# Performance work log

Measured on AMD Instinct MI355X. Metric: run time of the kernel, lower is better.

The kernel has to match this reference:

```python
import jax, jax.numpy as jnp
import numpy as np
from functools import partial

TOP_K = 2
LN_EPS = 1e-5


def setup_inputs() -> dict:
    key = jax.random.key(0)
    ks = jax.random.split(key, 4)
    B, T, H, F, E = 2, 2048, 1024, 4096, 8
    hidden_states = jax.random.normal(ks[0], (B, T, H), dtype=jnp.float32)
    # Router weights: original inits to zeros; use small random so routing is non-degenerate.
    router_w = jax.random.normal(ks[1], (E, H), dtype=jnp.float32) * 0.02
    router_b = jnp.zeros((E,), dtype=jnp.float32)
    W1 = jax.random.normal(ks[2], (E, H, F), dtype=jnp.float32) * (1.0 / np.sqrt(H))
    b1 = jnp.zeros((E, F), dtype=jnp.float32)
    W2 = jax.random.normal(ks[3], (E, F, H), dtype=jnp.float32) * (1.0 / np.sqrt(F))
    b2 = jnp.zeros((E, H), dtype=jnp.float32)
    ln_gamma = jnp.ones((H,), dtype=jnp.float32)
    ln_beta = jnp.zeros((H,), dtype=jnp.float32)
    return {"hidden_states": hidden_states, "router_w": router_w, "router_b": router_b,
            "W1": W1, "b1": b1, "W2": W2, "b2": b2,
            "ln_gamma": ln_gamma, "ln_beta": ln_beta}


def _layer_norm(x, gamma, beta):
    mu = jnp.mean(x, axis=-1, keepdims=True)
    var = jnp.var(x, axis=-1, keepdims=True)
    return (x - mu) * jax.lax.rsqrt(var + LN_EPS) * gamma + beta


def _moe_forward(hidden_states, router_w, router_b, W1, b1, W2, b2, ln_gamma, ln_beta):
    B, T, H = hidden_states.shape
    E = router_w.shape[0]
    N = B * T
    x = hidden_states.reshape(N, H)
    # Router (jitter=0.0, eval mode): logits [N, E]
    logits = x @ router_w.T + router_b
    topk_vals, topk_idx = jax.lax.top_k(logits, TOP_K)        # [N, K]
    topk_w = jax.nn.softmax(topk_vals, axis=-1)               # [N, K]
    # Scatter top-k weights into a dense combine matrix [N, E] (zeros elsewhere).
    probs = jnp.zeros((N, E), dtype=x.dtype).at[jnp.arange(N)[:, None], topk_idx].set(topk_w)
    # Per-expert FFN via scan over the (small, fixed) expert axis; each step is one
    # big GEMM over all tokens weighted by that expert's combine prob (0 for
    # tokens not routed to it) — same math as gather/MLP/scatter with no capacity drop.
    def body(acc, params_e):
        Wa, ba, Wb, bb, pe = params_e          # pe: [N]
        h = jax.nn.gelu(x @ Wa + ba, approximate=False)   # [N, F]
        y = h @ Wb + bb                                    # [N, H]
        return acc + y * pe[:, None], None
    out, _ = jax.lax.scan(body, jnp.zeros_like(x), (W1, b1, W2, b2, probs.T))
    out = out.reshape(B, T, H)
    return _layer_norm(out + hidden_states, ln_gamma, ln_beta)


def reference(hidden_states, router_w, router_b, W1, b1, W2, b2, ln_gamma, ln_beta):
    return _moe_forward(hidden_states, router_w, router_b, W1, b1, W2, b2, ln_gamma, ln_beta)
```

## Files before the change

### kernel.cpp

```cpp
#include <hip/hip_runtime.h>
#include <hip/hip_bf16.h>


typedef unsigned short u16;
typedef unsigned int u32;
typedef __attribute__((ext_vector_type(4))) float f32x4;
typedef __attribute__((ext_vector_type(8))) short s16x8;
typedef __attribute__((ext_vector_type(4))) unsigned short u16x4;
typedef __attribute__((ext_vector_type(8))) unsigned short u16x8;

#define GLD16(gp, lp) __builtin_amdgcn_global_load_lds( \
    (const __attribute__((address_space(1))) void*)(gp), \
    (__attribute__((address_space(3))) void*)(lp), 16, 0, 0)

__device__ __forceinline__ u16 f2bf(float f) {
    union { float f; u32 u; } v; v.f = f;
    u32 u = v.u;
    return (u16)((u + 0x7fffu + ((u >> 16) & 1u)) >> 16);
}
__device__ __forceinline__ float bf2f(u16 h) {
    union { u32 u; float f; } v; v.u = ((u32)h) << 16; return v.f;
}

__device__ __forceinline__ float gelu_f(float v) {
    const float u = v * (0.7978845608f + 0.0356774081f * v * v);
    const float t = __expf(-2.0f * u);
    return v * __builtin_amdgcn_rcpf(1.0f + t);
}

__global__ void k_init(int* cc) { if (threadIdx.x < 16) cc[threadIdx.x] = 0; }

__global__ __launch_bounds__(256) void k_pre(
    const float* __restrict__ x, const float* __restrict__ rw, const float* __restrict__ rb,
    u16* __restrict__ xb, int* __restrict__ eidx, float* __restrict__ wgt, int* __restrict__ counts,
    const float* __restrict__ W1, u16* __restrict__ W1t,
    const float* __restrict__ W2, u16* __restrict__ W2t)
{
    __shared__ u16 tl[256 * 128];
    const int id = blockIdx.x;
    const int tid = threadIdx.x;

    if (id >= 1024) {
        const float* s; u16* d; int R, C, r0, c0;
        if (id < 2048) {
            const int id2 = id - 1024;
            const int e = id2 >> 7, rem = id2 & 127;
            const int rt = rem >> 5, ct = rem & 31;
            s = W1 + (size_t)e * 1024 * 4096; d = W1t + (size_t)e * 1024 * 4096;
            R = 1024; C = 4096; r0 = rt * 256; c0 = ct * 128;
        } else {
            const int id3 = id - 2048;
            const int e = id3 >> 7, rem = id3 & 127;
            const int rt = rem >> 3, ct = rem & 7;
            s = W2 + (size_t)e * 4096 * 1024; d = W2t + (size_t)e * 4096 * 1024;
            R = 4096; C = 1024; r0 = rt * 256; c0 = ct * 128;
        }
        const int g = tid >> 5, ln = tid & 31;
        #pragma unroll 4
        for (int it = 0; it < 32; ++it) {
            const int r = it * 8 + g;
            const float4 v = *(const float4*)(s + (size_t)(r0 + r) * C + c0 + ln * 4);
            u16x4 pk;
            pk[0] = f2bf(v.x); pk[1] = f2bf(v.y); pk[2] = f2bf(v.z); pk[3] = f2bf(v.w);
            const int word = r * 32 + (ln ^ (r >> 3));
            *(u16x4*)(&tl[word * 4]) = pk;
        }
        __syncthreads();
        #pragma unroll 2
        for (int it = 0; it < 16; ++it) {
            const int c = it * 8 + g;
            const int cw = c >> 2, ce = c & 3;
            u16x8 o;
            #pragma unroll
            for (int j = 0; j < 8; ++j) {
                const int r = ln * 8 + j;
                const int word = r * 32 + (cw ^ (r >> 3));
                o[j] = tl[word * 4 + ce];
            }
            *(u16x8*)(d + (size_t)(c0 + c) * R + r0 + ln * 8) = o;
        }
        return;
    }

    const int wav = tid >> 6, lane = tid & 63;
    const int t = id * 4 + wav;
    const float* xt = x + (size_t)t * 1024;
    float acc[8] = {0.f,0.f,0.f,0.f,0.f,0.f,0.f,0.f};
    #pragma unroll
    for (int c = 0; c < 4; c++) {
        const int base = c * 256 + lane * 4;
        const float4 xv = *(const float4*)(xt + base);
        ushort4 pk;
        pk.x = f2bf(xv.x); pk.y = f2bf(xv.y); pk.z = f2bf(xv.z); pk.w = f2bf(xv.w);
        *(ushort4*)(xb + (size_t)t * 1024 + base) = pk;
        #pragma unroll
        for (int e = 0; e < 8; e++) {
            const float4 wv = *(const float4*)(rw + e * 1024 + base);
            acc[e] += xv.x * wv.x + xv.y * wv.y + xv.z * wv.z + xv.w * wv.w;
        }
    }
    #pragma unroll
    for (int e = 0; e < 8; e++) {
        #pragma unroll
        for (int s = 32; s; s >>= 1) acc[e] += __shfl_xor(acc[e], s);
    }
    if (lane == 0) {
        float v0 = -3e38f, v1 = -3e38f; int i0 = 0, i1 = 0;
        #pragma unroll
        for (int e = 0; e < 8; e++) {
            const float l = acc[e] + rb[e];
            if (l > v0) { v1 = v0; i1 = i0; v0 = l; i0 = e; }
            else if (l > v1) { v1 = l; i1 = e; }
        }
        const float w0 = 1.0f / (1.0f + expf(v1 - v0));
        eidx[2 * t] = i0; eidx[2 * t + 1] = i1;
        wgt[2 * t] = w0; wgt[2 * t + 1] = 1.0f - w0;
        atomicAdd(&counts[i0], 1); atomicAdd(&counts[i1], 1);
    }
}

__global__ __launch_bounds__(256) void k_place2(
    const int* __restrict__ eidx, const int* __restrict__ counts, int* __restrict__ cursors,
    int* __restrict__ offsets, int* __restrict__ rows, int* __restrict__ pos_of)
{
    int base[8];
    int s = 0;
    #pragma unroll
    for (int e = 0; e < 8; e++) { base[e] = s; s += counts[e]; }
    if (blockIdx.x == 0 && threadIdx.x == 0) {
        #pragma unroll
        for (int e = 0; e < 8; e++) offsets[e] = base[e];
        offsets[8] = s;
    }
    const int a = blockIdx.x * 256 + threadIdx.x;
    const int e = eidx[a];
    const int pos = base[e] + atomicAdd(&cursors[e], 1);
    rows[pos] = a >> 1;
    pos_of[a] = pos;
}

#define STAGE_T(b, k0) { \
    char* ad = (char*)At + (b) * 8192 + wav * 1024; \
    char* bd = (char*)Bt + (b) * 8192 + wav * 1024; \
    GLD16(a_src0 + (k0), ad); \
    GLD16(a_src1 + (k0), ad + 4096); \
    GLD16(b_src0 + (k0), bd); \
    GLD16(b_src1 + (k0), bd + 4096); }

#define COMPUTE_T(b) { \
    const u16* Abp = Ab + (b) * 4096; \
    const u16* Bbp = Bb + (b) * 4096; \
    s16x8 af[4], bfr[4]; \
    _Pragma("unroll") \
    for (int i = 0; i < 4; i++) { \
        af[i]  = *(const s16x8*)(Abp + i * 512); \
        bfr[i] = *(const s16x8*)(Bbp + i * 512); \
    } \
    __builtin_amdgcn_s_setprio(1); \
    _Pragma("unroll") \
    for (int mi = 0; mi < 4; mi++) \
        _Pragma("unroll") \
        for (int ni = 0; ni < 4; ni++) \
            acc[mi][ni] = __builtin_amdgcn_mfma_f32_16x16x32_bf16(af[mi], bfr[ni], acc[mi][ni], 0, 0, 0); \
    __builtin_amdgcn_s_setprio(0); }

#define VMCNT4 asm volatile("s_waitcnt vmcnt(4)" ::: "memory")
#define VMCNT0 asm volatile("s_waitcnt vmcnt(0)" ::: "memory")
#define BAR __builtin_amdgcn_s_barrier()

__global__ __launch_bounds__(256, 4) void k_gemm1(
    const u16* __restrict__ xb, const u16* __restrict__ W1t, const float* __restrict__ b1,
    u16* __restrict__ hbuf, const int* __restrict__ rows, const int* __restrict__ offsets)
{
    const int fid = blockIdx.x;
    const int swz = (fid & 7) * 1024 + (fid >> 3);
    const int y = swz & 31, xx = (swz >> 5) & 31, e = swz >> 10;

    const int off = offsets[e], cnt = offsets[e + 1] - off;
    const int row0 = y * 128;
    if (row0 >= cnt) return;
    const int n0 = xx * 128;
    const int tid = threadIdx.x;
    const int lane = tid & 63, wav = tid >> 6, lane15 = lane & 15;

    __shared__ u16 At[2][128][32];
    __shared__ u16 Bt[2][128][32];

    const int ar0 = tid >> 2;
    const int cl8 = (((tid & 3) ^ ((tid >> 3) & 3))) * 8;
    const int t0 = rows[off + min(row0 + ar0, cnt - 1)];
    const int t1 = rows[off + min(row0 + ar0 + 64, cnt - 1)];
    const u16* a_src0 = xb + (size_t)t0 * 1024 + cl8;
    const u16* a_src1 = xb + (size_t)t1 * 1024 + cl8;
    const u16* b_src0 = W1t + ((size_t)e * 4096 + n0 + ar0) * 1024 + cl8;
    const u16* b_src1 = b_src0 + (size_t)64 * 1024;

    f32x4 acc[4][4] = {};
    const int wr = wav >> 1, wc = wav & 1;
    const int koff = ((lane >> 4) ^ ((lane >> 1) & 3)) * 8;
    const u16* Ab = &At[0][wr * 64 + lane15][koff];
    const u16* Bb = &Bt[0][wc * 64 + lane15][koff];

    STAGE_T(0, 0);
    int b = 0;
    for (int k0 = 32; k0 < 1024; k0 += 32) {
        STAGE_T(b ^ 1, k0);
        VMCNT4;
        BAR;
        COMPUTE_T(b);
        BAR;
        b ^= 1;
    }
    VMCNT0;
    BAR;
    COMPUTE_T(b);

    const int rb4 = (lane >> 4) * 4;
    const int colbase = n0 + wc * 64 + lane15;
    float bias[4];
    #pragma unroll
    for (int ni = 0; ni < 4; ni++) bias[ni] = b1[e * 4096 + colbase + ni * 16];
    #pragma unroll
    for (int mi = 0; mi < 4; mi++) {
        #pragma unroll
        for (int j = 0; j < 4; j++) {
            const int lrow = wr * 64 + mi * 16 + rb4 + j;
            if (row0 + lrow < cnt) {
                const size_t gr = (size_t)(off + row0 + lrow);
                #pragma unroll
                for (int ni = 0; ni < 4; ni++) {
                    const float v = acc[mi][ni][j] + bias[ni];
                    hbuf[gr * 4096 + colbase + ni * 16] = f2bf(gelu_f(v));
                }
            }
        }
    }
}

__global__ __launch_bounds__(256, 4) void k_gemm2(
    const u16* __restrict__ hbuf, const u16* __restrict__ W2t, const float* __restrict__ b2,
    u16* __restrict__ yb, const int* __restrict__ offsets)
{
    const int fid = blockIdx.x;
    const int swz = (fid & 7) * 1024 + (fid >> 3);
    const int y = swz & 31, xx = (swz >> 5) & 7, z = swz >> 8;
    const int e = z >> 2, kq = z & 3;

    const int off = offsets[e], cnt = offsets[e + 1] - off;
    const int row0 = y * 128;
    if (row0 >= cnt) return;
    const int n0 = xx * 128;
    const int tid = threadIdx.x;
    const int lane = tid & 63, wav = tid >> 6, lane15 = lane & 15;
    const int kbase = kq * 1024;

    __shared__ u16 At[2][128][32];
    __shared__ u16 Bt[2][128][32];

    const int ar0 = tid >> 2;
    const int cl8 = (((tid & 3) ^ ((tid >> 3) & 3))) * 8;
    const u16* a_src0 = hbuf + (size_t)(off + min(row0 + ar0, cnt - 1)) * 4096 + kbase + cl8;
    const u16* a_src1 = hbuf + (size_t)(off + min(row0 + ar0 + 64, cnt - 1)) * 4096 + kbase + cl8;
    const u16* b_src0 = W2t + ((size_t)e * 1024 + n0 + ar0) * 4096 + kbase + cl8;
    const u16* b_src1 = b_src0 + (size_t)64 * 4096;

    f32x4 acc[4][4] = {};
    const int wr = wav >> 1, wc = wav & 1;
    const int koff = ((lane >> 4) ^ ((lane >> 1) & 3)) * 8;
    const u16* Ab = &At[0][wr * 64 + lane15][koff];
    const u16* Bb = &Bt[0][wc * 64 + lane15][koff];

    STAGE_T(0, 0);
    int b = 0;
    for (int k0 = 32; k0 < 1024; k0 += 32) {
        STAGE_T(b ^ 1, k0);
        VMCNT4;
        BAR;
        COMPUTE_T(b);
        BAR;
        b ^= 1;
    }
    VMCNT0;
    BAR;
    COMPUTE_T(b);

    u16* yy = yb + (size_t)kq * 8192 * 1024;
    const int rb4 = (lane >> 4) * 4;
    const int colbase = n0 + wc * 64 + lane15;
    float bias[4];
    #pragma unroll
    for (int ni = 0; ni < 4; ni++) bias[ni] = (kq == 0) ? b2[e * 1024 + colbase + ni * 16] : 0.f;
    #pragma unroll
    for (int mi = 0; mi < 4; mi++) {
        #pragma unroll
        for (int j = 0; j < 4; j++) {
            const int lrow = wr * 64 + mi * 16 + rb4 + j;
            if (row0 + lrow < cnt) {
                const size_t gr = (size_t)(off + row0 + lrow);
                #pragma unroll
                for (int ni = 0; ni < 4; ni++)
                    yy[gr * 1024 + colbase + ni * 16] = f2bf(acc[mi][ni][j] + bias[ni]);
            }
        }
    }
}

__global__ __launch_bounds__(256) void k_combine(
    const float* __restrict__ x, const u16* __restrict__ yb,
    const int* __restrict__ pos_of, const float* __restrict__ wgt,
    const float* __restrict__ gamma, const float* __restrict__ beta,
    float* __restrict__ out)
{
    const int t = blockIdx.x;
    const int tid = threadIdx.x;
    const int p0 = pos_of[2 * t], p1 = pos_of[2 * t + 1];
    const float w0 = wgt[2 * t], w1 = wgt[2 * t + 1];
    const int j4 = tid * 4;
    const float4 xv = *(const float4*)(x + (size_t)t * 1024 + j4);
    float s0[4] = {0.f, 0.f, 0.f, 0.f};
    float s1[4] = {0.f, 0.f, 0.f, 0.f};
    #pragma unroll
    for (int kq = 0; kq < 4; kq++) {
        const u16* ybq = yb + (size_t)kq * 8192 * 1024;
        const ushort4 u0 = *(const ushort4*)(ybq + (size_t)p0 * 1024 + j4);
        const ushort4 u1 = *(const ushort4*)(ybq + (size_t)p1 * 1024 + j4);
        s0[0] += bf2f(u0.x); s0[1] += bf2f(u0.y); s0[2] += bf2f(u0.z); s0[3] += bf2f(u0.w);
        s1[0] += bf2f(u1.x); s1[1] += bf2f(u1.y); s1[2] += bf2f(u1.z); s1[3] += bf2f(u1.w);
    }
    float a0 = xv.x + w0 * s0[0] + w1 * s1[0];
    float a1 = xv.y + w0 * s0[1] + w1 * s1[1];
    float a2 = xv.z + w0 * s0[2] + w1 * s1[2];
    float a3 = xv.w + w0 * s0[3] + w1 * s1[3];
    float s = a0 + a1 + a2 + a3;
    float q = a0 * a0 + a1 * a1 + a2 * a2 + a3 * a3;
    #pragma unroll
    for (int o = 32; o; o >>= 1) { s += __shfl_xor(s, o); q += __shfl_xor(q, o); }
    __shared__ float ls[4], lq[4];
    const int wav = tid >> 6, lane = tid & 63;
    if (lane == 0) { ls[wav] = s; lq[wav] = q; }
    __syncthreads();
    s = ls[0] + ls[1] + ls[2] + ls[3];
    q = lq[0] + lq[1] + lq[2] + lq[3];
    const float mu = s * (1.0f / 1024.0f);
    const float var = q * (1.0f / 1024.0f) - mu * mu;
    const float rs = rsqrtf(var + 1e-5f);
    const float4 g = *(const float4*)(gamma + j4);
    const float4 b = *(const float4*)(beta + j4);
    float4 o4;
    o4.x = (a0 - mu) * rs * g.x + b.x;
    o4.y = (a1 - mu) * rs * g.y + b.y;
    o4.z = (a2 - mu) * rs * g.z + b.z;
    o4.w = (a3 - mu) * rs * g.w + b.w;
    *(float4*)(out + (size_t)t * 1024 + j4) = o4;
}

extern "C" void kernel_launch(void* const* d_in, const int* in_sizes, int n_in,
                              void* d_out, int out_size, void* d_ws, size_t ws_size,
                              hipStream_t stream) {
    const float* x     = (const float*)d_in[0];
    const float* rw    = (const float*)d_in[1];
    const float* rb    = (const float*)d_in[2];
    const float* W1    = (const float*)d_in[3];
    const float* b1    = (const float*)d_in[4];
    const float* W2    = (const float*)d_in[5];
    const float* b2    = (const float*)d_in[6];
    const float* gamma = (const float*)d_in[7];
    const float* beta  = (const float*)d_in[8];
    float* out = (float*)d_out;

    char* p = (char*)d_ws;
    auto alloc = [&](size_t bytes) { char* r = p; p += (bytes + 255) & ~(size_t)255; return r; };
    int*   counts  = (int*)alloc(16 * sizeof(int));
    int*   cursors = counts + 8;
    int*   offsets = (int*)alloc(9 * sizeof(int));
    int*   eidx    = (int*)alloc(8192 * sizeof(int));
    float* wgt     = (float*)alloc(8192 * sizeof(float));
    int*   pos_of  = (int*)alloc(8192 * sizeof(int));
    int*   rows    = (int*)alloc(8192 * sizeof(int));
    u16*   xb      = (u16*)alloc((size_t)4096 * 1024 * 2);
    u16*   W1t     = (u16*)alloc((size_t)8 * 4096 * 1024 * 2);
    u16*   W2t     = (u16*)alloc((size_t)8 * 1024 * 4096 * 2);
    u16*   hbuf    = (u16*)alloc((size_t)8192 * 4096 * 2);
    u16* yb = W1t;

    hipLaunchKernelGGL(k_init, dim3(1), dim3(64), 0, stream, counts);
    hipLaunchKernelGGL(k_pre, dim3(3072), dim3(256), 0, stream,
                       x, rw, rb, xb, eidx, wgt, counts, W1, W1t, W2, W2t);
    hipLaunchKernelGGL(k_place2, dim3(32), dim3(256), 0, stream,
                       eidx, counts, cursors, offsets, rows, pos_of);
    hipLaunchKernelGGL(k_gemm1, dim3(8192), dim3(256), 0, stream, xb, W1t, b1, hbuf, rows, offsets);
    hipLaunchKernelGGL(k_gemm2, dim3(8192), dim3(256), 0, stream, hbuf, W2t, b2, yb, offsets);
    hipLaunchKernelGGL(k_combine, dim3(4096), dim3(256), 0, stream, x, yb, pos_of, wgt, gamma, beta, out);
}
```

Measured before the change: 428.3 us.

## Move W2 transpose into GEMM1 launch and drop LDS from weight transposes

The W2 fp32-to-bf16 transpose moves out of the preprocessing kernel and into extra leading blocks of the first GEMM launch, so it can overlap with GEMM1 compute. Both weight transposes now use a register-only scheme: each thread reads 8 strided fp32 values down a column and writes one 16-byte bf16 vector, with no shared-memory staging or barrier. The aim is to hide transpose memory traffic and cut LDS use and barriers. The risk is that the strided per-thread reads are less coalesced, and the transpose blocks compete with GEMM blocks for CUs.

Measured after the change: 449.4 us. +4.9%, slower.

```diff
diff --git a/kernel.cpp b/kernel.cpp
--- a/kernel.cpp
+++ b/kernel.cpp
@@ -6,7 +6,6 @@
 typedef unsigned int u32;
 typedef __attribute__((ext_vector_type(4))) float f32x4;
 typedef __attribute__((ext_vector_type(8))) short s16x8;
-typedef __attribute__((ext_vector_type(4))) unsigned short u16x4;
 typedef __attribute__((ext_vector_type(8))) unsigned short u16x8;
 
 #define GLD16(gp, lp) __builtin_amdgcn_global_load_lds( \
@@ -30,55 +29,38 @@
 
 __global__ void k_init(int* cc) { if (threadIdx.x < 16) cc[threadIdx.x] = 0; }
 
+__device__ __forceinline__ void transp_nolds(
+    const float* __restrict__ s, u16* __restrict__ d, int K, int N, int n0, int k0, int tid)
+{
+    const int n = n0 + tid;
+    #pragma unroll 4
+    for (int c8 = 0; c8 < 8; ++c8) {
+        const int kb = k0 + c8 * 8;
+        float v[8];
+        #pragma unroll
+        for (int j = 0; j < 8; ++j)
+            v[j] = s[(size_t)(kb + j) * N + n];
+        u16x8 o;
+        #pragma unroll
+        for (int j = 0; j < 8; ++j) o[j] = f2bf(v[j]);
+        *(u16x8*)(d + (size_t)n * K + kb) = o;
+    }
+}
+
 __global__ __launch_bounds__(256) void k_pre(
     const float* __restrict__ x, const float* __restrict__ rw, const float* __restrict__ rb,
     u16* __restrict__ xb, int* __restrict__ eidx, float* __restrict__ wgt, int* __restrict__ counts,
-    const float* __restrict__ W1, u16* __restrict__ W1t,
-    const float* __restrict__ W2, u16* __restrict__ W2t)
-{
-    __shared__ u16 tl[256 * 128];
+    const float* __restrict__ W1, u16* __restrict__ W1t)
+{
     const int id = blockIdx.x;
     const int tid = threadIdx.x;
 
     if (id >= 1024) {
-        const float* s; u16* d; int R, C, r0, c0;
-        if (id < 2048) {
-            const int id2 = id - 1024;
-            const int e = id2 >> 7, rem = id2 & 127;
-            const int rt = rem >> 5, ct = rem & 31;
-            s = W1 + (size_t)e * 1024 * 4096; d = W1t + (size_t)e * 1024 * 4096;
-            R = 1024; C = 4096; r0 = rt * 256; c0 = ct * 128;
-        } else {
-            const int id3 = id - 2048;
-            const int e = id3 >> 7, rem = id3 & 127;
-            const int rt = rem >> 3, ct = rem & 7;
-            s = W2 + (size_t)e * 4096 * 1024; d = W2t + (size_t)e * 4096 * 1024;
-            R = 4096; C = 1024; r0 = rt * 256; c0 = ct * 128;
-        }
-        const int g = tid >> 5, ln = tid & 31;
-        #pragma unroll 4
-        for (int it = 0; it < 32; ++it) {
-            const int r = it * 8 + g;
-            const float4 v = *(const float4*)(s + (size_t)(r0 + r) * C + c0 + ln * 4);
-            u16x4 pk;
-            pk[0] = f2bf(v.x); pk[1] = f2bf(v.y); pk[2] = f2bf(v.z); pk[3] = f2bf(v.w);
-            const int word = r * 32 + (ln ^ (r >> 3));
-            *(u16x4*)(&tl[word * 4]) = pk;
-        }
-        __syncthreads();
-        #pragma unroll 2
-        for (int it = 0; it < 16; ++it) {
-            const int c = it * 8 + g;
-            const int cw = c >> 2, ce = c & 3;
-            u16x8 o;
-            #pragma unroll
-            for (int j = 0; j < 8; ++j) {
-                const int r = ln * 8 + j;
-                const int word = r * 32 + (cw ^ (r >> 3));
-                o[j] = tl[word * 4 + ce];
-            }
-            *(u16x8*)(d + (size_t)(c0 + c) * R + r0 + ln * 8) = o;
-        }
+        const int id2 = id - 1024;
+        const int e = id2 >> 8, rem = id2 & 255;
+        const int nb = rem >> 4, kc = rem & 15;
+        transp_nolds(W1 + (size_t)e * 1024 * 4096, W1t + (size_t)e * 1024 * 4096,
+                     1024, 4096, nb * 256, kc * 64, tid);
         return;
     }
 
@@ -168,11 +150,23 @@
 #define VMCNT0 asm volatile("s_waitcnt vmcnt(0)" ::: "memory")
 #define BAR __builtin_amdgcn_s_barrier()
 
-__global__ __launch_bounds__(256, 4) void k_gemm1(
+__global__ __launch_bounds__(256, 4) void k_gemm1f(
     const u16* __restrict__ xb, const u16* __restrict__ W1t, const float* __restrict__ b1,
-    u16* __restrict__ hbuf, const int* __restrict__ rows, const int* __restrict__ offsets)
-{
-    const int fid = blockIdx.x;
+    u16* __restrict__ hbuf, const int* __restrict__ rows, const int* __restrict__ offsets,
+    const float* __restrict__ W2, u16* __restrict__ W2t)
+{
+    const int bid = blockIdx.x;
+    const int tid = threadIdx.x;
+
+    if (bid < 2048) {
+        const int e = bid >> 8, rem = bid & 255;
+        const int nb = rem >> 6, kc = rem & 63;
+        transp_nolds(W2 + (size_t)e * 4096 * 1024, W2t + (size_t)e * 1024 * 4096,
+                     4096, 1024, nb * 256, kc * 64, tid);
+        return;
+    }
+
+    const int fid = bid - 2048;
     const int swz = (fid & 7) * 1024 + (fid >> 3);
     const int y = swz & 31, xx = (swz >> 5) & 31, e = swz >> 10;
 
@@ -180,7 +174,6 @@
     const int row0 = y * 128;
     if (row0 >= cnt) return;
     const int n0 = xx * 128;
-    const int tid = threadIdx.x;
     const int lane = tid & 63, wav = tid >> 6, lane15 = lane & 15;
 
     __shared__ u16 At[2][128][32];
@@ -385,10 +378,11 @@
 
     hipLaunchKernelGGL(k_init, dim3(1), dim3(64), 0, stream, counts);
     hipLaunchKernelGGL(k_pre, dim3(3072), dim3(256), 0, stream,
-                       x, rw, rb, xb, eidx, wgt, counts, W1, W1t, W2, W2t);
+                       x, rw, rb, xb, eidx, wgt, counts, W1, W1t);
     hipLaunchKernelGGL(k_place2, dim3(32), dim3(256), 0, stream,
                        eidx, counts, cursors, offsets, rows, pos_of);
-    hipLaunchKernelGGL(k_gemm1, dim3(8192), dim3(256), 0, stream, xb, W1t, b1, hbuf, rows, offsets);
+    hipLaunchKernelGGL(k_gemm1f, dim3(10240), dim3(256), 0, stream,
+                       xb, W1t, b1, hbuf, rows, offsets, W2, W2t);
     hipLaunchKernelGGL(k_gemm2, dim3(8192), dim3(256), 0, stream, hbuf, W2t, b2, yb, offsets);
     hipLaunchKernelGGL(k_combine, dim3(4096), dim3(256), 0, stream, x, yb, pos_of, wgt, gamma, beta, out);
 }
```
